# Optimization experiments

Hardware: AMD Instinct MI355X
Metric: run time of the kernel (lower is better)

## Reference

```python
import jax, jax.numpy as jnp
import numpy as np

B, S, D, E, H, F, L, C = 32768, 5, 512, 256, 4, 2048, 2, 5  # batch, sensors, input_dim, embed_dim, heads, ffn, layers, classes
DH = E // H
EPS = 1e-5


def layer_norm(x, g, b):
    m = jnp.mean(x, axis=-1, keepdims=True)
    v = jnp.mean((x - m) ** 2, axis=-1, keepdims=True)
    return (x - m) * jax.lax.rsqrt(v + EPS) * g + b


def setup_inputs() -> dict:
    key = jax.random.key(0)
    ks = jax.random.split(key, 24)
    n = lambda k, shape: (jax.random.normal(k, shape, dtype=jnp.float32) * 0.02)
    return {
        "x": jax.random.normal(ks[0], (B, S, D), dtype=jnp.float32),
        "sensor_types": jax.random.randint(ks[1], (B, S), 0, 2, dtype=jnp.int32),
        "gps_w": n(ks[2], (E, D)), "gps_b": jnp.zeros((E,), jnp.float32),
        "ang_w": n(ks[3], (E, D)), "ang_b": jnp.zeros((E,), jnp.float32),
        "qkv_w": n(ks[4], (L, 3 * E, E)), "qkv_b": jnp.zeros((L, 3 * E), jnp.float32),
        "attn_ow": n(ks[5], (L, E, E)), "attn_ob": jnp.zeros((L, E), jnp.float32),
        "ln1_g": jnp.ones((L, E), jnp.float32), "ln1_b": jnp.zeros((L, E), jnp.float32),
        "ff1_w": n(ks[6], (L, F, E)), "ff1_b": jnp.zeros((L, F), jnp.float32),
        "ff2_w": n(ks[7], (L, E, F)), "ff2_b": jnp.zeros((L, E), jnp.float32),
        "ln2_g": jnp.ones((L, E), jnp.float32), "ln2_b": jnp.zeros((L, E), jnp.float32),
        "fc1_w": n(ks[8], (128, S * E)), "fc1_b": jnp.zeros((128,), jnp.float32),
        "fc2_w": n(ks[9], (64, 128)), "fc2_b": jnp.zeros((64,), jnp.float32),
        "out_w": n(ks[10], (C, 64)), "out_b": jnp.zeros((C,), jnp.float32),
    }


def reference(x, sensor_types, gps_w, gps_b, ang_w, ang_b, qkv_w, qkv_b,
              attn_ow, attn_ob, ln1_g, ln1_b, ff1_w, ff1_b, ff2_w, ff2_b,
              ln2_g, ln2_b, fc1_w, fc1_b, fc2_w, fc2_b, out_w, out_b):
    # Dual-expert routing: compute both branches, blend by mask (same math as masked scatter)
    is_gps = (sensor_types == 0)[..., None]  # [B,S,1]
    g = jax.nn.relu(jnp.einsum('bsd,ed->bse', x, gps_w) + gps_b)
    a = jax.nn.relu(jnp.einsum('bsd,ed->bse', x, ang_w) + ang_b)
    h = jnp.where(is_gps, g, a)  # [B,S,E]

    # TransformerEncoder (post-LN, ReLU FFN, dropout inactive at eval)
    for l in range(L):
        qkv = jnp.einsum('bse,fe->bsf', h, qkv_w[l]) + qkv_b[l]  # [B,S,3E]
        q, k, v = jnp.split(qkv, 3, axis=-1)
        q = q.reshape(B, S, H, DH); k = k.reshape(B, S, H, DH); v = v.reshape(B, S, H, DH)
        scores = jnp.einsum('bqhd,bkhd->bhqk', q, k) / jnp.sqrt(jnp.float32(DH))
        attn = jax.nn.softmax(scores, axis=-1)
        o = jnp.einsum('bhqk,bkhd->bqhd', attn, v).reshape(B, S, E)
        o = o @ attn_ow[l].T + attn_ob[l]
        h = layer_norm(h + o, ln1_g[l], ln1_b[l])
        ff = jax.nn.relu(h @ ff1_w[l].T + ff1_b[l]) @ ff2_w[l].T + ff2_b[l]
        h = layer_norm(h + ff, ln2_g[l], ln2_b[l])

    z = h.reshape(B, S * E)
    z = z @ fc1_w.T + fc1_b
    z = z @ fc2_w.T + fc2_b
    return z @ out_w.T + out_b
```

## Files before the change

### kernel.cpp

```cpp
#include <hip/hip_runtime.h>


#define N_TOK 163840
#define NBATCH 32768

typedef __attribute__((ext_vector_type(8))) short bfrag;
typedef __attribute__((ext_vector_type(4))) float f32x4;

__device__ __forceinline__ float bf2f(ushort u) {
  return __builtin_bit_cast(float, (uint)u << 16);
}
__device__ __forceinline__ ushort f2bf(float f) {
  uint u = __builtin_bit_cast(uint, f);
  return (ushort)((u + 0x7FFFu + ((u >> 16) & 1u)) >> 16);
}

__global__ __launch_bounds__(256) void cvt_kernel(const float* __restrict__ in,
                                                  ushort* __restrict__ out, int n4) {
  int i = blockIdx.x * 256 + threadIdx.x;
  if (i >= n4) return;
  float4 v = ((const float4*)in)[i];
  ushort4 o;
  o.x = f2bf(v.x); o.y = f2bf(v.y); o.z = f2bf(v.z); o.w = f2bf(v.w);
  ((ushort4*)out)[i] = o;
}

enum { EPI_F32 = 0, EPI_F32_RELU = 1, EPI_BF16 = 2, EPI_BF16_RELU = 3, EPI_SELECT = 4 };

template <int EPI>
__global__ __launch_bounds__(256) void gemm_bt(const ushort* __restrict__ A,
                                               const ushort* __restrict__ W,
                                               const float* __restrict__ bias,
                                               void* __restrict__ outp,
                                               int M, int K, int O,
                                               const float* __restrict__ gbuf,
                                               const int* __restrict__ stype,
                                               ushort* __restrict__ h16out) {
  __shared__ ushort As[128][32];
  __shared__ ushort Bs[128][32];
  const int tid = threadIdx.x;
  const int wave = tid >> 6, lane = tid & 63;
  const int bm = blockIdx.y, bn = blockIdx.x;
  const int wm = (wave & 1) << 6, wn = (wave >> 1) << 6;
  const int srow = tid >> 2;
  const int sq   = tid & 3;
  const int sc   = ((sq ^ ((srow >> 2) & 3))) << 3;
  const int scol = sq << 3;

  const ushort* Abase = A + (size_t)(bm * 128 + srow) * K + scol;
  const ushort* Wbase = W + (size_t)(bn * 128 + srow) * K + scol;

  f32x4 acc[4][4];
#pragma unroll
  for (int i = 0; i < 4; i++)
#pragma unroll
    for (int j = 0; j < 4; j++) acc[i][j] = {0.f, 0.f, 0.f, 0.f};

  const int fr = lane & 15;
  const int fq = lane >> 4;
  const int rc = (fq ^ ((fr >> 2) & 3)) << 3;

  uint4 a0 = *(const uint4*)(Abase);
  uint4 a1 = *(const uint4*)(Abase + (size_t)64 * K);
  uint4 b0 = *(const uint4*)(Wbase);
  uint4 b1 = *(const uint4*)(Wbase + (size_t)64 * K);

  for (int k0 = 0; k0 < K; k0 += 32) {
    *(uint4*)&As[srow][sc]      = a0;
    *(uint4*)&As[srow + 64][sc] = a1;
    *(uint4*)&Bs[srow][sc]      = b0;
    *(uint4*)&Bs[srow + 64][sc] = b1;
    __syncthreads();
    if (k0 + 32 < K) {
      a0 = *(const uint4*)(Abase + k0 + 32);
      a1 = *(const uint4*)(Abase + k0 + 32 + (size_t)64 * K);
      b0 = *(const uint4*)(Wbase + k0 + 32);
      b1 = *(const uint4*)(Wbase + k0 + 32 + (size_t)64 * K);
    }
    bfrag af[4], bf_[4];
#pragma unroll
    for (int i = 0; i < 4; i++) af[i] = *(const bfrag*)&As[wm + i * 16 + fr][rc];
#pragma unroll
    for (int j = 0; j < 4; j++) bf_[j] = *(const bfrag*)&Bs[wn + j * 16 + fr][rc];
#pragma unroll
    for (int i = 0; i < 4; i++)
#pragma unroll
      for (int j = 0; j < 4; j++)
        acc[i][j] = __builtin_amdgcn_mfma_f32_16x16x32_bf16(af[i], bf_[j], acc[i][j], 0, 0, 0);
    __syncthreads();
  }

  const int cr = fq << 2;
  const int cc = fr;
#pragma unroll
  for (int j = 0; j < 4; j++) {
    const int col = bn * 128 + wn + j * 16 + cc;
    const float bv = bias[col];
#pragma unroll
    for (int i = 0; i < 4; i++) {
      const int row = bm * 128 + wm + i * 16 + cr;
#pragma unroll
      for (int r = 0; r < 4; r++) {
        float v = acc[i][j][r] + bv;
        const size_t idx = (size_t)(row + r) * O + col;
        if (EPI != EPI_F32 && EPI != EPI_BF16) v = fmaxf(v, 0.f);
        if (EPI == EPI_SELECT) {
          if (stype[row + r] == 0) v = gbuf[idx];
          ((float*)outp)[idx] = v;
          h16out[idx] = f2bf(v);
        } else if (EPI == EPI_F32 || EPI == EPI_F32_RELU) {
          ((float*)outp)[idx] = v;
        } else {
          ((ushort*)outp)[idx] = f2bf(v);
        }
      }
    }
  }
}

__global__ __launch_bounds__(512) void gemm_lnres(const ushort* __restrict__ A,
                                                  const ushort* __restrict__ W,
                                                  const float* __restrict__ bias,
                                                  float* __restrict__ h32,
                                                  ushort* __restrict__ h16,
                                                  const float* __restrict__ g,
                                                  const float* __restrict__ b,
                                                  int K) {
  __shared__ ushort As[128][32];
  __shared__ ushort Bs[256][32];
  __shared__ float2 s_part[128][4];
  __shared__ float2 s_mr[128];
  const int tid = threadIdx.x;
  const int wave = tid >> 6, lane = tid & 63;
  const int bm = blockIdx.x;
  const int wm = (wave & 1) << 6, wn = (wave >> 1) << 6;

  const int srow = tid >> 2;
  const int sq   = tid & 3;
  const int sc   = ((sq ^ ((srow >> 2) & 3))) << 3;
  const int scol = sq << 3;
  const ushort* Ag = A + (size_t)(bm * 128 + srow) * K + scol;
  const ushort* Wg = W + (size_t)srow * K + scol;

  f32x4 acc[4][4];
#pragma unroll
  for (int i = 0; i < 4; i++)
#pragma unroll
    for (int j = 0; j < 4; j++) acc[i][j] = {0.f, 0.f, 0.f, 0.f};

  const int fr = lane & 15;
  const int fq = lane >> 4;
  const int rc = (fq ^ ((fr >> 2) & 3)) << 3;

  uint4 a0 = *(const uint4*)(Ag);
  uint4 b0 = *(const uint4*)(Wg);
  uint4 b1 = *(const uint4*)(Wg + (size_t)128 * K);

  for (int k0 = 0; k0 < K; k0 += 32) {
    *(uint4*)&As[srow][sc]       = a0;
    *(uint4*)&Bs[srow][sc]       = b0;
    *(uint4*)&Bs[srow + 128][sc] = b1;
    __syncthreads();
    if (k0 + 32 < K) {
      a0 = *(const uint4*)(Ag + k0 + 32);
      b0 = *(const uint4*)(Wg + k0 + 32);
      b1 = *(const uint4*)(Wg + k0 + 32 + (size_t)128 * K);
    }
    bfrag af[4], bf_[4];
#pragma unroll
    for (int i = 0; i < 4; i++) af[i] = *(const bfrag*)&As[wm + i * 16 + fr][rc];
#pragma unroll
    for (int j = 0; j < 4; j++) bf_[j] = *(const bfrag*)&Bs[wn + j * 16 + fr][rc];
#pragma unroll
    for (int i = 0; i < 4; i++)
#pragma unroll
      for (int j = 0; j < 4; j++)
        acc[i][j] = __builtin_amdgcn_mfma_f32_16x16x32_bf16(af[i], bf_[j], acc[i][j], 0, 0, 0);
    __syncthreads();
  }

  const int cr = fq << 2;
  const int cc = fr;
#pragma unroll
  for (int i = 0; i < 4; i++) {
#pragma unroll
    for (int r = 0; r < 4; r++) {
      const int row = wm + i * 16 + cr + r;
      const size_t grow = (size_t)(bm * 128 + row) * 256;
      float s = 0.f, sq2 = 0.f;
#pragma unroll
      for (int j = 0; j < 4; j++) {
        const int col = wn + j * 16 + cc;
        float u = acc[i][j][r] + bias[col] + h32[grow + col];
        acc[i][j][r] = u;
        s += u; sq2 += u * u;
      }
#pragma unroll
      for (int o = 1; o < 16; o <<= 1) { s += __shfl_xor(s, o); sq2 += __shfl_xor(sq2, o); }
      if ((lane & 15) == 0) s_part[row][wave >> 1] = {s, sq2};
    }
  }
  __syncthreads();
  if (tid < 128) {
    float2 p0 = s_part[tid][0], p1 = s_part[tid][1], p2 = s_part[tid][2], p3 = s_part[tid][3];
    float S = p0.x + p1.x + p2.x + p3.x;
    float SQ = p0.y + p1.y + p2.y + p3.y;
    float mean = S * 0.00390625f;
    float var = SQ * 0.00390625f - mean * mean;
    s_mr[tid] = {mean, rsqrtf(var + 1e-5f)};
  }
  __syncthreads();
#pragma unroll
  for (int i = 0; i < 4; i++) {
#pragma unroll
    for (int r = 0; r < 4; r++) {
      const int row = wm + i * 16 + cr + r;
      const float2 mr = s_mr[row];
      const size_t grow = (size_t)(bm * 128 + row) * 256;
#pragma unroll
      for (int j = 0; j < 4; j++) {
        const int col = wn + j * 16 + cc;
        float y = (acc[i][j][r] - mr.x) * mr.y * g[col] + b[col];
        h32[grow + col] = y;
        h16[grow + col] = f2bf(y);
      }
    }
  }
}

__global__ __launch_bounds__(512) void ffn_fused(const ushort* __restrict__ h16in,
                                                 const ushort* __restrict__ W1,
                                                 const float* __restrict__ b1,
                                                 const ushort* __restrict__ W2,
                                                 const float* __restrict__ b2,
                                                 float* __restrict__ h32,
                                                 ushort* __restrict__ h16out,
                                                 const float* __restrict__ g,
                                                 const float* __restrict__ bb) {
  __shared__ ushort sh[128][264];
  __shared__ ushort smid[128][136];
  __shared__ float2 s_part[128][4];
  __shared__ float2 s_mr[128];
  const int tid = threadIdx.x;
  const int wave = tid >> 6, lane = tid & 63;
  const size_t tok0 = (size_t)blockIdx.x * 128;

  {
    const int r = tid >> 2, c0 = (tid & 3) << 6;
    const ushort* src = h16in + (tok0 + r) * 256 + c0;
#pragma unroll
    for (int u = 0; u < 8; u++)
      *(uint4*)&sh[r][c0 + u * 8] = *(const uint4*)(src + u * 8);
  }

  const int fr = lane & 15;
  const int fq = lane >> 4;
  const int cr = fq << 2;
  const int cc = fr;
  const int tm = (wave & 1) << 6;
  const int mq = (wave >> 1) << 5;
  const int oq = (wave >> 1) << 6;

  f32x4 acc2[4][4];
#pragma unroll
  for (int i = 0; i < 4; i++)
#pragma unroll
    for (int j = 0; j < 4; j++) acc2[i][j] = {0.f, 0.f, 0.f, 0.f};

  __syncthreads();

  for (int c = 0; c < 16; c++) {
    f32x4 acc1[4][2];
#pragma unroll
    for (int i = 0; i < 4; i++)
#pragma unroll
      for (int j = 0; j < 2; j++) acc1[i][j] = {0.f, 0.f, 0.f, 0.f};
#pragma unroll 2
    for (int k = 0; k < 8; k++) {
      const int ko = k * 32 + fq * 8;
      bfrag af[4], bf_[2];
#pragma unroll
      for (int i = 0; i < 4; i++) af[i] = *(const bfrag*)&sh[tm + i * 16 + fr][ko];
#pragma unroll
      for (int j = 0; j < 2; j++)
        bf_[j] = *(const bfrag*)(W1 + (size_t)(c * 128 + mq + j * 16 + fr) * 256 + ko);
#pragma unroll
      for (int i = 0; i < 4; i++)
#pragma unroll
        for (int j = 0; j < 2; j++)
          acc1[i][j] = __builtin_amdgcn_mfma_f32_16x16x32_bf16(af[i], bf_[j], acc1[i][j], 0, 0, 0);
    }
    __syncthreads();
#pragma unroll
    for (int j = 0; j < 2; j++) {
      const float bv = b1[c * 128 + mq + j * 16 + cc];
#pragma unroll
      for (int i = 0; i < 4; i++)
#pragma unroll
        for (int r = 0; r < 4; r++) {
          float v = fmaxf(acc1[i][j][r] + bv, 0.f);
          smid[tm + i * 16 + cr + r][mq + j * 16 + cc] = f2bf(v);
        }
    }
    __syncthreads();
#pragma unroll 2
    for (int k = 0; k < 4; k++) {
      const int ko = k * 32 + fq * 8;
      bfrag af[4], bf_[4];
#pragma unroll
      for (int i = 0; i < 4; i++) af[i] = *(const bfrag*)&smid[tm + i * 16 + fr][ko];
#pragma unroll
      for (int j = 0; j < 4; j++)
        bf_[j] = *(const bfrag*)(W2 + (size_t)(oq + j * 16 + fr) * 2048 + c * 128 + ko);
#pragma unroll
      for (int i = 0; i < 4; i++)
#pragma unroll
        for (int j = 0; j < 4; j++)
          acc2[i][j] = __builtin_amdgcn_mfma_f32_16x16x32_bf16(af[i], bf_[j], acc2[i][j], 0, 0, 0);
    }
  }

#pragma unroll
  for (int i = 0; i < 4; i++) {
#pragma unroll
    for (int r = 0; r < 4; r++) {
      const int row = tm + i * 16 + cr + r;
      const size_t grow = (tok0 + row) * 256;
      float s = 0.f, sq2 = 0.f;
#pragma unroll
      for (int j = 0; j < 4; j++) {
        const int col = oq + j * 16 + cc;
        float u = acc2[i][j][r] + b2[col] + h32[grow + col];
        acc2[i][j][r] = u;
        s += u; sq2 += u * u;
      }
#pragma unroll
      for (int o = 1; o < 16; o <<= 1) { s += __shfl_xor(s, o); sq2 += __shfl_xor(sq2, o); }
      if ((lane & 15) == 0) s_part[row][wave >> 1] = {s, sq2};
    }
  }
  __syncthreads();
  if (tid < 128) {
    float2 p0 = s_part[tid][0], p1 = s_part[tid][1], p2 = s_part[tid][2], p3 = s_part[tid][3];
    float S = p0.x + p1.x + p2.x + p3.x;
    float SQ = p0.y + p1.y + p2.y + p3.y;
    float mean = S * 0.00390625f;
    float var = SQ * 0.00390625f - mean * mean;
    s_mr[tid] = {mean, rsqrtf(var + 1e-5f)};
  }
  __syncthreads();
#pragma unroll
  for (int i = 0; i < 4; i++) {
#pragma unroll
    for (int r = 0; r < 4; r++) {
      const int row = tm + i * 16 + cr + r;
      const float2 mr = s_mr[row];
      const size_t grow = (tok0 + row) * 256;
#pragma unroll
      for (int j = 0; j < 4; j++) {
        const int col = oq + j * 16 + cc;
        float y = (acc2[i][j][r] - mr.x) * mr.y * g[col] + bb[col];
        h32[grow + col] = y;
        h16out[grow + col] = f2bf(y);
      }
    }
  }
}

__global__ __launch_bounds__(256) void attn_kernel(const ushort* __restrict__ qkv,
                                                   ushort* __restrict__ o16) {
  __shared__ ushort s_qkv[8 * 5 * 768];
  __shared__ float s_att[8 * 4 * 25];
  const int tid = threadIdx.x;
  const size_t gbase = (size_t)blockIdx.x * (8 * 5 * 768);
#pragma unroll
  for (int t = 0; t < 15; t++) {
    int i = tid + t * 256;
    *(uint4*)&s_qkv[i * 8] = *(const uint4*)(qkv + gbase + (size_t)i * 8);
  }
  __syncthreads();
  for (int idx = tid; idx < 800; idx += 256) {
    int b = idx / 100, r = idx - b * 100;
    int h = r / 25, ij = r - h * 25;
    int i = ij / 5, j = ij - i * 5;
    const ushort* qp = &s_qkv[(b * 5 + i) * 768 + h * 64];
    const ushort* kp = &s_qkv[(b * 5 + j) * 768 + 256 + h * 64];
    float s = 0.f;
#pragma unroll
    for (int d = 0; d < 64; d += 2) {
      uint qw = *(const uint*)&qp[d];
      uint kw = *(const uint*)&kp[d];
      s += bf2f((ushort)(qw & 0xffffu)) * bf2f((ushort)(kw & 0xffffu));
      s += bf2f((ushort)(qw >> 16)) * bf2f((ushort)(kw >> 16));
    }
    s_att[idx] = s * 0.125f;
  }
  __syncthreads();
  if (tid < 160) {
    float* sp = &s_att[tid * 5];
    float m = fmaxf(fmaxf(fmaxf(sp[0], sp[1]), fmaxf(sp[2], sp[3])), sp[4]);
    float e0 = __expf(sp[0] - m), e1 = __expf(sp[1] - m), e2 = __expf(sp[2] - m);
    float e3 = __expf(sp[3] - m), e4 = __expf(sp[4] - m);
    float inv = 1.f / (e0 + e1 + e2 + e3 + e4);
    sp[0] = e0 * inv; sp[1] = e1 * inv; sp[2] = e2 * inv; sp[3] = e3 * inv; sp[4] = e4 * inv;
  }
  __syncthreads();
  const size_t obase = (size_t)blockIdx.x * (8 * 5 * 256);
#pragma unroll
  for (int t = 0; t < 40; t++) {
    int idx = t * 256 + tid;
    int d = idx & 63;
    int rest = idx >> 6;
    int h = rest & 3; rest >>= 2;
    int i = rest % 5, b = rest / 5;
    const float* ap = &s_att[(b * 4 + h) * 25 + i * 5];
    const ushort* vp = &s_qkv[(b * 5) * 768 + 512 + h * 64 + d];
    float o = 0.f;
#pragma unroll
    for (int j = 0; j < 5; j++) o += ap[j] * bf2f(vp[j * 768]);
    o16[obase + (size_t)((b * 5 + i) * 256 + h * 64 + d)] = f2bf(o);
  }
}

__global__ __launch_bounds__(256) void head2_kernel(const float* __restrict__ z1,
                                                    const float* __restrict__ fc2w,
                                                    const float* __restrict__ fc2b,
                                                    const float* __restrict__ outw,
                                                    const float* __restrict__ outb,
                                                    float* __restrict__ out) {
  __shared__ float s_z2[4][64];
  const int wave = threadIdx.x >> 6, lane = threadIdx.x & 63;
  const int b = blockIdx.x * 4 + wave;
  const float* z = z1 + (size_t)b * 128;
  float acc = fc2b[lane];
#pragma unroll 8
  for (int k = 0; k < 128; k++) acc += z[k] * fc2w[lane * 128 + k];
  s_z2[wave][lane] = acc;
  __syncthreads();
  if (lane < 5) {
    const float* zz = s_z2[wave];
    float o = outb[lane];
#pragma unroll 8
    for (int k = 0; k < 64; k++) o += zz[k] * outw[lane * 64 + k];
    out[(size_t)b * 5 + lane] = o;
  }
}

extern "C" void kernel_launch(void* const* d_in, const int* in_sizes, int n_in,
                              void* d_out, int out_size, void* d_ws, size_t ws_size,
                              hipStream_t stream) {
  const float* x       = (const float*)d_in[0];
  const int*   stype   = (const int*)d_in[1];
  const float* gps_w   = (const float*)d_in[2];
  const float* gps_b   = (const float*)d_in[3];
  const float* ang_w   = (const float*)d_in[4];
  const float* ang_b   = (const float*)d_in[5];
  const float* qkv_w   = (const float*)d_in[6];
  const float* qkv_b   = (const float*)d_in[7];
  const float* attn_ow = (const float*)d_in[8];
  const float* attn_ob = (const float*)d_in[9];
  const float* ln1_g   = (const float*)d_in[10];
  const float* ln1_b   = (const float*)d_in[11];
  const float* ff1_w   = (const float*)d_in[12];
  const float* ff1_b   = (const float*)d_in[13];
  const float* ff2_w   = (const float*)d_in[14];
  const float* ff2_b   = (const float*)d_in[15];
  const float* ln2_g   = (const float*)d_in[16];
  const float* ln2_b   = (const float*)d_in[17];
  const float* fc1_w   = (const float*)d_in[18];
  const float* fc1_b   = (const float*)d_in[19];
  const float* fc2_w   = (const float*)d_in[20];
  const float* fc2_b   = (const float*)d_in[21];
  const float* out_w   = (const float*)d_in[22];
  const float* out_b   = (const float*)d_in[23];

  char* ws = (char*)d_ws;
  const size_t NEED = 763363328ull;
  if (ws_size < NEED) return;

  ushort* w_gps  = (ushort*)ws;
  ushort* w_ang  = w_gps + 131072;
  ushort* w_qkv  = w_ang + 131072;
  ushort* w_attn = w_qkv + 393216;
  ushort* w_ff1  = w_attn + 131072;
  ushort* w_ff2  = w_ff1 + 1048576;
  ushort* w_fc1  = w_ff2 + 1048576;

  ushort* R16 = (ushort*)(ws + (size_t)(8u << 20));
  ushort* h16 = (ushort*)(ws + 8388608ull + 251658240ull);
  float*  h32 = (float*)(ws + 8388608ull + 251658240ull + 83886080ull);
  float*  t32 = (float*)(ws + 8388608ull + 251658240ull + 83886080ull + 167772160ull);
  ushort* o16 = (ushort*)(ws + 8388608ull + 251658240ull + 83886080ull + 335544320ull);

  auto cvt = [&](const float* src, ushort* dst, int n4) {
    cvt_kernel<<<(n4 + 255) / 256, 256, 0, stream>>>(src, dst, n4);
  };
  cvt(gps_w, w_gps, 32768);
  cvt(ang_w, w_ang, 32768);
  cvt(qkv_w, w_qkv, 98304);
  cvt(attn_ow, w_attn, 32768);
  cvt(ff1_w, w_ff1, 262144);
  cvt(ff2_w, w_ff2, 262144);
  cvt(fc1_w, w_fc1, 40960);
  cvt(x, R16, 20971520);

  gemm_bt<EPI_F32_RELU><<<dim3(2, 1280), 256, 0, stream>>>(
      R16, w_gps, gps_b, t32, N_TOK, 512, 256, nullptr, nullptr, nullptr);
  gemm_bt<EPI_SELECT><<<dim3(2, 1280), 256, 0, stream>>>(
      R16, w_ang, ang_b, h32, N_TOK, 512, 256, t32, stype, h16);

  for (int l = 0; l < 2; l++) {
    gemm_bt<EPI_BF16><<<dim3(6, 1280), 256, 0, stream>>>(
        h16, w_qkv + l * 196608, qkv_b + l * 768, R16, N_TOK, 256, 768,
        nullptr, nullptr, nullptr);
    attn_kernel<<<4096, 256, 0, stream>>>(R16, o16);
    gemm_lnres<<<1280, 512, 0, stream>>>(o16, w_attn + l * 65536, attn_ob + l * 256,
                                         h32, h16, ln1_g + l * 256, ln1_b + l * 256, 256);
    ffn_fused<<<1280, 512, 0, stream>>>(h16, w_ff1 + l * 524288, ff1_b + l * 2048,
                                        w_ff2 + l * 524288, ff2_b + l * 256,
                                        h32, h16, ln2_g + l * 256, ln2_b + l * 256);
  }

  gemm_bt<EPI_F32><<<dim3(1, 256), 256, 0, stream>>>(
      h16, w_fc1, fc1_b, t32, NBATCH, 1280, 128, nullptr, nullptr, nullptr);
  head2_kernel<<<8192, 256, 0, stream>>>(t32, fc2_w, fc2_b, out_w, out_b, (float*)d_out);
}
```

Measured before the change: 3.387 ms.

## Shrink FFN tile to 64 tokens and software-prefetch weight fragments

The fused FFN kernel now handles 64 tokens per 256-thread block instead of 128 per 512-thread block, with launch_bounds(256,3) so more blocks fit per CU. W1 and W2 fragments are loaded one stage ahead, with the first k-slice of the next chunk prefetched during the current second GEMM. The k-loops are fully unrolled and MFMA sections are wrapped in s_setprio. This aims to hide global weight-load latency and raise occupancy. The cost is twice as many weight fetches per token and higher register pressure.

```diff
diff --git a/kernel.cpp b/kernel.cpp
--- a/kernel.cpp
+++ b/kernel.cpp
@@ -228,22 +228,22 @@
   }
 }
 
-__global__ __launch_bounds__(512) void ffn_fused(const ushort* __restrict__ h16in,
-                                                 const ushort* __restrict__ W1,
-                                                 const float* __restrict__ b1,
-                                                 const ushort* __restrict__ W2,
-                                                 const float* __restrict__ b2,
-                                                 float* __restrict__ h32,
-                                                 ushort* __restrict__ h16out,
-                                                 const float* __restrict__ g,
-                                                 const float* __restrict__ bb) {
-  __shared__ ushort sh[128][264];
-  __shared__ ushort smid[128][136];
-  __shared__ float2 s_part[128][4];
-  __shared__ float2 s_mr[128];
+__global__ __launch_bounds__(256, 3) void ffn_fused(const ushort* __restrict__ h16in,
+                                                    const ushort* __restrict__ W1,
+                                                    const float* __restrict__ b1,
+                                                    const ushort* __restrict__ W2,
+                                                    const float* __restrict__ b2,
+                                                    float* __restrict__ h32,
+                                                    ushort* __restrict__ h16out,
+                                                    const float* __restrict__ g,
+                                                    const float* __restrict__ bb) {
+  __shared__ ushort sh[64][264];
+  __shared__ ushort smid[64][136];
+  __shared__ float2 s_part[64][4];
+  __shared__ float2 s_mr[64];
   const int tid = threadIdx.x;
   const int wave = tid >> 6, lane = tid & 63;
-  const size_t tok0 = (size_t)blockIdx.x * 128;
+  const size_t tok0 = (size_t)blockIdx.x * 64;
 
   {
     const int r = tid >> 2, c0 = (tid & 3) << 6;
@@ -257,9 +257,11 @@
   const int fq = lane >> 4;
   const int cr = fq << 2;
   const int cc = fr;
-  const int tm = (wave & 1) << 6;
-  const int mq = (wave >> 1) << 5;
-  const int oq = (wave >> 1) << 6;
+  const int mq = wave << 5;
+  const int oq = wave << 6;
+
+  const ushort* w1p = W1 + (size_t)(mq + fr) * 256 + fq * 8;
+  const ushort* w2p = W2 + (size_t)(oq + fr) * 2048 + fq * 8;
 
   f32x4 acc2[4][4];
 #pragma unroll
@@ -267,29 +269,44 @@
 #pragma unroll
     for (int j = 0; j < 4; j++) acc2[i][j] = {0.f, 0.f, 0.f, 0.f};
 
+  bfrag nb1[2];
+  nb1[0] = *(const bfrag*)(w1p);
+  nb1[1] = *(const bfrag*)(w1p + 16 * 256);
+
   __syncthreads();
 
   for (int c = 0; c < 16; c++) {
+    const size_t c1 = (size_t)c * 32768;
     f32x4 acc1[4][2];
 #pragma unroll
     for (int i = 0; i < 4; i++)
 #pragma unroll
       for (int j = 0; j < 2; j++) acc1[i][j] = {0.f, 0.f, 0.f, 0.f};
-#pragma unroll 2
+#pragma unroll
     for (int k = 0; k < 8; k++) {
+      bfrag b1f[2];
+      if (k == 0) { b1f[0] = nb1[0]; b1f[1] = nb1[1]; }
+      else {
+        b1f[0] = *(const bfrag*)(w1p + c1 + k * 32);
+        b1f[1] = *(const bfrag*)(w1p + c1 + 16 * 256 + k * 32);
+      }
       const int ko = k * 32 + fq * 8;
-      bfrag af[4], bf_[2];
-#pragma unroll
-      for (int i = 0; i < 4; i++) af[i] = *(const bfrag*)&sh[tm + i * 16 + fr][ko];
-#pragma unroll
-      for (int j = 0; j < 2; j++)
-        bf_[j] = *(const bfrag*)(W1 + (size_t)(c * 128 + mq + j * 16 + fr) * 256 + ko);
+      bfrag af[4];
+#pragma unroll
+      for (int i = 0; i < 4; i++) af[i] = *(const bfrag*)&sh[i * 16 + fr][ko];
+      __builtin_amdgcn_s_setprio(1);
 #pragma unroll
       for (int i = 0; i < 4; i++)
 #pragma unroll
         for (int j = 0; j < 2; j++)
-          acc1[i][j] = __builtin_amdgcn_mfma_f32_16x16x32_bf16(af[i], bf_[j], acc1[i][j], 0, 0, 0);
-    }
+          acc1[i][j] = __builtin_amdgcn_mfma_f32_16x16x32_bf16(af[i], b1f[j], acc1[i][j], 0, 0, 0);
+      __builtin_amdgcn_s_setprio(0);
+    }
+    bfrag nb2[4];
+#pragma unroll
+    for (int j = 0; j < 4; j++)
+      nb2[j] = *(const bfrag*)(w2p + (size_t)j * 32768 + c * 128);
+
     __syncthreads();
 #pragma unroll
     for (int j = 0; j < 2; j++) {
@@ -299,24 +316,34 @@
 #pragma unroll
         for (int r = 0; r < 4; r++) {
           float v = fmaxf(acc1[i][j][r] + bv, 0.f);
-          smid[tm + i * 16 + cr + r][mq + j * 16 + cc] = f2bf(v);
+          smid[i * 16 + cr + r][mq + j * 16 + cc] = f2bf(v);
         }
     }
     __syncthreads();
-#pragma unroll 2
+#pragma unroll
     for (int k = 0; k < 4; k++) {
+      bfrag b2f[4];
+      if (k == 0) {
+        b2f[0] = nb2[0]; b2f[1] = nb2[1]; b2f[2] = nb2[2]; b2f[3] = nb2[3];
+        const size_t cn = (size_t)((c + 1) & 15) * 32768;
+        nb1[0] = *(const bfrag*)(w1p + cn);
+        nb1[1] = *(const bfrag*)(w1p + cn + 16 * 256);
+      } else {
+#pragma unroll
+        for (int j = 0; j < 4; j++)
+          b2f[j] = *(const bfrag*)(w2p + (size_t)j * 32768 + c * 128 + k * 32);
+      }
       const int ko = k * 32 + fq * 8;
-      bfrag af[4], bf_[4];
-#pragma unroll
-      for (int i = 0; i < 4; i++) af[i] = *(const bfrag*)&smid[tm + i * 16 + fr][ko];
-#pragma unroll
-      for (int j = 0; j < 4; j++)
-        bf_[j] = *(const bfrag*)(W2 + (size_t)(oq + j * 16 + fr) * 2048 + c * 128 + ko);
+      bfrag af[4];
+#pragma unroll
+      for (int i = 0; i < 4; i++) af[i] = *(const bfrag*)&smid[i * 16 + fr][ko];
+      __builtin_amdgcn_s_setprio(1);
 #pragma unroll
       for (int i = 0; i < 4; i++)
 #pragma unroll
         for (int j = 0; j < 4; j++)
-          acc2[i][j] = __builtin_amdgcn_mfma_f32_16x16x32_bf16(af[i], bf_[j], acc2[i][j], 0, 0, 0);
+          acc2[i][j] = __builtin_amdgcn_mfma_f32_16x16x32_bf16(af[i], b2f[j], acc2[i][j], 0, 0, 0);
+      __builtin_amdgcn_s_setprio(0);
     }
   }
 
@@ -324,7 +351,7 @@
   for (int i = 0; i < 4; i++) {
 #pragma unroll
     for (int r = 0; r < 4; r++) {
-      const int row = tm + i * 16 + cr + r;
+      const int row = i * 16 + cr + r;
       const size_t grow = (tok0 + row) * 256;
       float s = 0.f, sq2 = 0.f;
 #pragma unroll
@@ -336,11 +363,11 @@
       }
 #pragma unroll
       for (int o = 1; o < 16; o <<= 1) { s += __shfl_xor(s, o); sq2 += __shfl_xor(sq2, o); }
-      if ((lane & 15) == 0) s_part[row][wave >> 1] = {s, sq2};
-    }
-  }
-  __syncthreads();
-  if (tid < 128) {
+      if ((lane & 15) == 0) s_part[row][wave] = {s, sq2};
+    }
+  }
+  __syncthreads();
+  if (tid < 64) {
     float2 p0 = s_part[tid][0], p1 = s_part[tid][1], p2 = s_part[tid][2], p3 = s_part[tid][3];
     float S = p0.x + p1.x + p2.x + p3.x;
     float SQ = p0.y + p1.y + p2.y + p3.y;
@@ -353,7 +380,7 @@
   for (int i = 0; i < 4; i++) {
 #pragma unroll
     for (int r = 0; r < 4; r++) {
-      const int row = tm + i * 16 + cr + r;
+      const int row = i * 16 + cr + r;
       const float2 mr = s_mr[row];
       const size_t grow = (tok0 + row) * 256;
 #pragma unroll
@@ -516,7 +543,7 @@
     attn_kernel<<<4096, 256, 0, stream>>>(R16, o16);
     gemm_lnres<<<1280, 512, 0, stream>>>(o16, w_attn + l * 65536, attn_ob + l * 256,
                                          h32, h16, ln1_g + l * 256, ln1_b + l * 256, 256);
-    ffn_fused<<<1280, 512, 0, stream>>>(h16, w_ff1 + l * 524288, ff1_b + l * 2048,
+    ffn_fused<<<2560, 256, 0, stream>>>(h16, w_ff1 + l * 524288, ff1_b + l * 2048,
                                         w_ff2 + l * 524288, ff2_b + l * 256,
                                         h32, h16, ln2_g + l * 256, ln2_b + l * 256);
   }
```

Result: no change. 3.391 ms (+0.1%).
